# Optimization experiments

Measured on AMD Instinct MI355X. Metric: run time of the kernel, lower is better.

The kernel has to match this reference:

```python
import jax, jax.numpy as jnp
import numpy as np

C = 64          # number of concepts (output_size)
MC = 100        # num_monte_carlo
TRI = C * (C + 1) // 2
ROWS, COLS = np.tril_indices(C)          # static lower-triangular indices
DIAG_MASK = ROWS == COLS                 # positions in c_sigma that are diagonal
DIAG = np.arange(C)


def setup_inputs() -> dict:
    key = jax.random.key(0)
    k_x, k_eps, k_wmu, k_wsig = jax.random.split(key, 4)
    B, F = 4096, 512
    return {
        "x": jax.random.normal(k_x, (B, F), jnp.float32),
        "eps": jax.random.normal(k_eps, (B, C, MC), jnp.float32),  # MVN standard-normal draws
        "w_mu": jax.random.normal(k_wmu, (C, F), jnp.float32) / np.float32(np.sqrt(F)),
        "b_mu": jnp.zeros((C,), jnp.float32),
        # sigma.weight.data *= 0.01 in the original module
        "w_sigma": jax.random.normal(k_wsig, (TRI, F), jnp.float32) * np.float32(0.01 / np.sqrt(F)),
        "b_sigma": jnp.zeros((TRI,), jnp.float32),
    }


def reference(x, eps, w_mu, b_mu, w_sigma, b_sigma):
    # mu head: Linear(F -> C)
    c_mu = x @ w_mu.T + b_mu                          # [B, C]
    # sigma head: Linear(F -> C*(C+1)/2)
    c_sigma = x @ w_sigma.T + b_sigma                 # [B, TRI]

    B = x.shape[0]
    # build lower-triangular scale matrix (predict_sigma)
    L = jnp.zeros((B, C, C), x.dtype)
    L = L.at[:, ROWS, COLS].set(c_sigma)
    diag_vals = jax.nn.softplus(c_sigma[:, DIAG_MASK]) + 1e-6
    L = L.at[:, DIAG, DIAG].set(diag_vals)            # [B, C, C]

    # MVN rsample([MC]) with scale_tril L: sample = mu + L @ eps
    logits = c_mu[:, :, None] + jnp.einsum('bij,bjm->bim', L, eps)  # [B, C, MC]
    return jax.nn.sigmoid(logits)
```

## Files before the change

kernel.cpp:

```cpp
#include <hip/hip_runtime.h>
#include <hip/hip_bf16.h>


typedef short bf16x8 __attribute__((ext_vector_type(8)));
typedef float f32x4 __attribute__((ext_vector_type(4)));

__device__ __forceinline__ unsigned short f2bf(float f) {
    union { float f; unsigned u; } u; u.f = f;
    unsigned r = u.u + 0x7FFFu + ((u.u >> 16) & 1u);
    return (unsigned short)(r >> 16);
}

__device__ __forceinline__ void tri_ij(int t, int& i, int& j) {
    i = (int)((sqrtf((float)(8 * t + 1)) - 1.0f) * 0.5f);
    if ((i + 1) * (i + 2) / 2 <= t) ++i;
    if (i * (i + 1) / 2 > t) --i;
    j = t - ((i * (i + 1)) >> 1);
}

__device__ __forceinline__ void gload16(const void* g, void* l) {
    __builtin_amdgcn_global_load_lds(
        (const __attribute__((address_space(1))) void*)g,
        (__attribute__((address_space(3))) void*)l, 16, 0, 0);
}

__global__ __launch_bounds__(256) void cvt_kernel(
    const float* __restrict__ x, const float* __restrict__ wmu,
    const float* __restrict__ wsig,
    unsigned short* __restrict__ Xb, unsigned short* __restrict__ Wb,
    uint4* __restrict__ Ldz) {
    const int NX = (4096 * 512) / 4;
    const int NW = (2144 * 512) / 4;
    const int NMU = (64 * 512) / 4;
    const int NZ = (4096 * 64 * 64 * 2) / 16;
    int tot = NX + NW + NZ;
    for (int i = blockIdx.x * blockDim.x + threadIdx.x; i < tot;
         i += gridDim.x * blockDim.x) {
        if (i < NX + NW) {
            float4 v; unsigned short* dst;
            if (i < NX) {
                v = ((const float4*)x)[i];
                dst = Xb + (size_t)i * 4;
            } else {
                int j = i - NX;
                if (j < NMU) v = ((const float4*)wmu)[j];
                else         v = ((const float4*)wsig)[j - NMU];
                dst = Wb + (size_t)j * 4;
            }
            ushort4 o;
            o.x = f2bf(v.x); o.y = f2bf(v.y); o.z = f2bf(v.z); o.w = f2bf(v.w);
            *(ushort4*)dst = o;
        } else {
            Ldz[i - NX - NW] = make_uint4(0u, 0u, 0u, 0u);
        }
    }
}

__global__ __launch_bounds__(256) void gemm_kernel(
    const unsigned short* __restrict__ Xb, const unsigned short* __restrict__ Wb,
    const float* __restrict__ bmu, const float* __restrict__ bsig,
    float* __restrict__ Mu, unsigned short* __restrict__ Ld) {
    __shared__ __align__(16) unsigned short smem[16384];

    int flat = blockIdx.y * 17 + blockIdx.x;
    int virt = (flat & 7) * 68 + (flat >> 3);
    int vbx = virt % 17, vby = virt / 17;
    int r0 = vby * 128, c0 = vbx * 128;

    int tid = threadIdx.x;
    int w = tid >> 6, lane = tid & 63;
    int wr = w >> 1, wc = w & 1;
    int lr = lane & 15, kg = lane >> 4;

    int sr = tid >> 3;
    int sc = tid & 7;
    int scx = sc ^ (sr & 7);
    const unsigned short* Ag = Xb + (size_t)(r0 + sr) * 512 + scx * 8;
    const unsigned short* Bg = Wb + (size_t)(c0 + sr) * 512 + scx * 8;
    unsigned short* As = smem + tid * 8;
    unsigned short* Bs = smem + 8192 + tid * 8;

    f32x4 acc[4][4];
    #pragma unroll
    for (int i = 0; i < 4; ++i)
        #pragma unroll
        for (int j = 0; j < 4; ++j) acc[i][j] = (f32x4){0.f, 0.f, 0.f, 0.f};

    for (int kt = 0; kt < 8; ++kt) {
        int k0 = kt * 64;
        #pragma unroll
        for (int i = 0; i < 4; ++i) {
            gload16(Ag + (size_t)i * 32 * 512 + k0, As + i * 2048);
            gload16(Bg + (size_t)i * 32 * 512 + k0, Bs + i * 2048);
        }
        __syncthreads();
        #pragma unroll
        for (int h = 0; h < 2; ++h) {
            bf16x8 a[4], bv[4];
            #pragma unroll
            for (int i = 0; i < 4; ++i) {
                int row = wr * 64 + i * 16 + lr;
                int ch = ((h << 2) | kg) ^ (row & 7);
                a[i] = *(const bf16x8*)(smem + row * 64 + ch * 8);
            }
            #pragma unroll
            for (int j = 0; j < 4; ++j) {
                int row = wc * 64 + j * 16 + lr;
                int ch = ((h << 2) | kg) ^ (row & 7);
                bv[j] = *(const bf16x8*)(smem + 8192 + row * 64 + ch * 8);
            }
            #pragma unroll
            for (int i = 0; i < 4; ++i)
                #pragma unroll
                for (int j = 0; j < 4; ++j)
                    acc[i][j] = __builtin_amdgcn_mfma_f32_16x16x32_bf16(
                        a[i], bv[j], acc[i][j], 0, 0, 0);
        }
        __syncthreads();
    }

    int rbase = r0 + wr * 64 + (kg << 2);
    #pragma unroll
    for (int j = 0; j < 4; ++j) {
        int col = c0 + wc * 64 + j * 16 + lr;
        if (col < 64) {
            float bias = bmu[col];
            #pragma unroll
            for (int i = 0; i < 4; ++i)
                #pragma unroll
                for (int r = 0; r < 4; ++r)
                    Mu[(size_t)(rbase + i * 16 + r) * 64 + col] = acc[i][j][r] + bias;
        } else if (col < 2144) {
            int t = col - 64;
            float bias = bsig[t];
            int ti, tj; tri_ij(t, ti, tj);
            bool dg = (tj == ti);
            int ofs = ti * 64 + tj;
            #pragma unroll
            for (int i = 0; i < 4; ++i) {
                #pragma unroll
                for (int r = 0; r < 4; ++r) {
                    float v = acc[i][j][r] + bias;
                    if (dg) v = (v > 15.f ? v : __logf(1.f + __expf(v))) + 1e-6f;
                    Ld[((size_t)(rbase + i * 16 + r) << 12) + ofs] = f2bf(v);
                }
            }
        }
    }
}

__global__ __launch_bounds__(512, 4) void sample_kernel(
    const float* __restrict__ Mu, const unsigned short* __restrict__ Ld,
    const float* __restrict__ eps, float* __restrict__ out) {
    __shared__ __align__(16) float Ost[6400];

    int b = blockIdx.x;
    int tid = threadIdx.x;
    int w = tid >> 6, lane = tid & 63;
    int lr = lane & 15, kg = lane >> 4;
    int m = (w << 4) + lr;
    int ml = (m < 100) ? m : 96;
    int m0 = (w << 4) + (kg << 2);
    bool cw = (w < 7);
    bool st = cw && (m0 < 100);

    if (cw) {
        const float* er = eps + (size_t)b * 6400;
        float ef[16];
        #pragma unroll
        for (int s = 0; s < 8; ++s) {
            ef[s]     = er[(kg * 8 + s) * 100 + ml];
            ef[s + 8] = er[(32 + kg * 8 + s) * 100 + ml];
        }
        float muv[4];
        #pragma unroll
        for (int g = 0; g < 4; ++g)
            muv[g] = Mu[((size_t)b << 6) + g * 16 + lr];
        bf16x8 a0, a1;
        #pragma unroll
        for (int s = 0; s < 4; ++s) {
            __hip_bfloat162 h0 = __float22bfloat162_rn(
                make_float2(ef[2 * s], ef[2 * s + 1]));
            __hip_bfloat162 h1 = __float22bfloat162_rn(
                make_float2(ef[8 + 2 * s], ef[8 + 2 * s + 1]));
            ((unsigned*)&a0)[s] = *(unsigned*)&h0;
            ((unsigned*)&a1)[s] = *(unsigned*)&h1;
        }
        const unsigned short* lb = Ld + ((size_t)b << 12);
        #pragma unroll
        for (int g = 0; g < 4; ++g) {
            int i = g * 16 + lr;
            bf16x8 L0 = *(const bf16x8*)(lb + i * 64 + kg * 8);
            bf16x8 L1 = *(const bf16x8*)(lb + i * 64 + (kg + 4) * 8);
            f32x4 acc = {0.f, 0.f, 0.f, 0.f};
            acc = __builtin_amdgcn_mfma_f32_16x16x32_bf16(a0, L0, acc, 0, 0, 0);
            acc = __builtin_amdgcn_mfma_f32_16x16x32_bf16(a1, L1, acc, 0, 0, 0);
            if (st) {
                float4 o;
                #pragma unroll
                for (int r = 0; r < 4; ++r) {
                    float z = muv[g] + acc[r];
                    ((float*)&o)[r] = __fdividef(1.f, 1.f + __expf(-z));
                }
                *(float4*)&Ost[i * 100 + m0] = o;
            }
        }
    }

    __syncthreads();

    size_t ob = (size_t)b * 6400;
    #pragma unroll
    for (int kk = 0; kk < 4; ++kk) {
        int f = tid + (kk << 9);
        if (f < 1600)
            *(float4*)(out + ob + f * 4) = ((const float4*)Ost)[f];
    }
}

extern "C" void kernel_launch(void* const* d_in, const int* in_sizes, int n_in,
                              void* d_out, int out_size, void* d_ws, size_t ws_size,
                              hipStream_t stream) {
    const float* x    = (const float*)d_in[0];
    const float* eps  = (const float*)d_in[1];
    const float* wmu  = (const float*)d_in[2];
    const float* bmu  = (const float*)d_in[3];
    const float* wsig = (const float*)d_in[4];
    const float* bsig = (const float*)d_in[5];
    float* out = (float*)d_out;

    char* ws = (char*)d_ws;
    unsigned short* Xb = (unsigned short*)ws;
    unsigned short* Wb = (unsigned short*)(ws + 4194304);
    float*          Mu = (float*)(ws + 4194304 + 2195456);
    unsigned short* Ld = (unsigned short*)(ws + 7438336);

    cvt_kernel<<<2048, 256, 0, stream>>>(x, wmu, wsig, Xb, Wb, (uint4*)Ld);
    gemm_kernel<<<dim3(17, 32), 256, 0, stream>>>(Xb, Wb, bmu, bsig, Mu, Ld);
    sample_kernel<<<4096, 512, 0, stream>>>(Mu, Ld, eps, out);
}
```

Baseline: 94.58 us.

## Store packed triangular sigma and build L in LDS, batch four rows per block

Drops the dense zero-initialised 64x64 bf16 L buffer and instead writes the packed triangular sigma (2080 values per row) from the GEMM. The sample kernel stages the packed sigma and eps into LDS and expands L into MFMA fragments with masked reads. Each block now handles four batch rows in sequence with a swizzled grid mapping, which cuts the zero-fill and the dense L traffic. The costs are more LDS use, lower occupancy, and serial per-row loops with extra barriers.

```diff
diff --git a/kernel.cpp b/kernel.cpp
--- a/kernel.cpp
+++ b/kernel.cpp
@@ -10,6 +10,8 @@
     unsigned r = u.u + 0x7FFFu + ((u.u >> 16) & 1u);
     return (unsigned short)(r >> 16);
 }
+
+__device__ __forceinline__ int swz(int r) { return (r ^ (r >> 3)) & 7; }
 
 __device__ __forceinline__ void tri_ij(int t, int& i, int& j) {
     i = (int)((sqrtf((float)(8 * t + 1)) - 1.0f) * 0.5f);
@@ -27,39 +29,33 @@
 __global__ __launch_bounds__(256) void cvt_kernel(
     const float* __restrict__ x, const float* __restrict__ wmu,
     const float* __restrict__ wsig,
-    unsigned short* __restrict__ Xb, unsigned short* __restrict__ Wb,
-    uint4* __restrict__ Ldz) {
+    unsigned short* __restrict__ Xb, unsigned short* __restrict__ Wb) {
     const int NX = (4096 * 512) / 4;
     const int NW = (2144 * 512) / 4;
     const int NMU = (64 * 512) / 4;
-    const int NZ = (4096 * 64 * 64 * 2) / 16;
-    int tot = NX + NW + NZ;
+    int tot = NX + NW;
     for (int i = blockIdx.x * blockDim.x + threadIdx.x; i < tot;
          i += gridDim.x * blockDim.x) {
-        if (i < NX + NW) {
-            float4 v; unsigned short* dst;
-            if (i < NX) {
-                v = ((const float4*)x)[i];
-                dst = Xb + (size_t)i * 4;
-            } else {
-                int j = i - NX;
-                if (j < NMU) v = ((const float4*)wmu)[j];
-                else         v = ((const float4*)wsig)[j - NMU];
-                dst = Wb + (size_t)j * 4;
-            }
-            ushort4 o;
-            o.x = f2bf(v.x); o.y = f2bf(v.y); o.z = f2bf(v.z); o.w = f2bf(v.w);
-            *(ushort4*)dst = o;
+        float4 v; unsigned short* dst;
+        if (i < NX) {
+            v = ((const float4*)x)[i];
+            dst = Xb + (size_t)i * 4;
         } else {
-            Ldz[i - NX - NW] = make_uint4(0u, 0u, 0u, 0u);
-        }
+            int j = i - NX;
+            if (j < NMU) v = ((const float4*)wmu)[j];
+            else         v = ((const float4*)wsig)[j - NMU];
+            dst = Wb + (size_t)j * 4;
+        }
+        ushort4 o;
+        o.x = f2bf(v.x); o.y = f2bf(v.y); o.z = f2bf(v.z); o.w = f2bf(v.w);
+        *(ushort4*)dst = o;
     }
 }
 
 __global__ __launch_bounds__(256) void gemm_kernel(
     const unsigned short* __restrict__ Xb, const unsigned short* __restrict__ Wb,
     const float* __restrict__ bmu, const float* __restrict__ bsig,
-    float* __restrict__ Mu, unsigned short* __restrict__ Ld) {
+    float* __restrict__ Mu, unsigned short* __restrict__ Sg) {
     __shared__ __align__(16) unsigned short smem[16384];
 
     int flat = blockIdx.y * 17 + blockIdx.x;
@@ -135,86 +131,120 @@
             float bias = bsig[t];
             int ti, tj; tri_ij(t, ti, tj);
             bool dg = (tj == ti);
-            int ofs = ti * 64 + tj;
             #pragma unroll
             for (int i = 0; i < 4; ++i) {
                 #pragma unroll
                 for (int r = 0; r < 4; ++r) {
                     float v = acc[i][j][r] + bias;
                     if (dg) v = (v > 15.f ? v : __logf(1.f + __expf(v))) + 1e-6f;
-                    Ld[((size_t)(rbase + i * 16 + r) << 12) + ofs] = f2bf(v);
+                    Sg[(size_t)(rbase + i * 16 + r) * 2080 + t] = f2bf(v);
                 }
             }
         }
     }
 }
 
-__global__ __launch_bounds__(512, 4) void sample_kernel(
-    const float* __restrict__ Mu, const unsigned short* __restrict__ Ld,
+__global__ __launch_bounds__(512, 3) void sample_kernel(
+    const float* __restrict__ Mu, const unsigned short* __restrict__ Sg,
     const float* __restrict__ eps, float* __restrict__ out) {
+    __shared__ __align__(16) unsigned short EpT[112][64];
+    __shared__ __align__(16) unsigned short Sgs[2080];
     __shared__ __align__(16) float Ost[6400];
 
-    int b = blockIdx.x;
+    int flat = blockIdx.x;
+    int virt = (flat & 7) * 128 + (flat >> 3);
+    int b0 = virt << 2;
+
     int tid = threadIdx.x;
     int w = tid >> 6, lane = tid & 63;
     int lr = lane & 15, kg = lane >> 4;
-    int m = (w << 4) + lr;
-    int ml = (m < 100) ? m : 96;
+    bool cw = (w < 7);
     int m0 = (w << 4) + (kg << 2);
-    bool cw = (w < 7);
     bool st = cw && (m0 < 100);
-
-    if (cw) {
-        const float* er = eps + (size_t)b * 6400;
-        float ef[16];
-        #pragma unroll
-        for (int s = 0; s < 8; ++s) {
-            ef[s]     = er[(kg * 8 + s) * 100 + ml];
-            ef[s + 8] = er[(32 + kg * 8 + s) * 100 + ml];
-        }
-        float muv[4];
-        #pragma unroll
-        for (int g = 0; g < 4; ++g)
-            muv[g] = Mu[((size_t)b << 6) + g * 16 + lr];
-        bf16x8 a0, a1;
-        #pragma unroll
-        for (int s = 0; s < 4; ++s) {
-            __hip_bfloat162 h0 = __float22bfloat162_rn(
-                make_float2(ef[2 * s], ef[2 * s + 1]));
-            __hip_bfloat162 h1 = __float22bfloat162_rn(
-                make_float2(ef[8 + 2 * s], ef[8 + 2 * s + 1]));
-            ((unsigned*)&a0)[s] = *(unsigned*)&h0;
-            ((unsigned*)&a1)[s] = *(unsigned*)&h1;
-        }
-        const unsigned short* lb = Ld + ((size_t)b << 12);
-        #pragma unroll
-        for (int g = 0; g < 4; ++g) {
-            int i = g * 16 + lr;
-            bf16x8 L0 = *(const bf16x8*)(lb + i * 64 + kg * 8);
-            bf16x8 L1 = *(const bf16x8*)(lb + i * 64 + (kg + 4) * 8);
-            f32x4 acc = {0.f, 0.f, 0.f, 0.f};
-            acc = __builtin_amdgcn_mfma_f32_16x16x32_bf16(a0, L0, acc, 0, 0, 0);
-            acc = __builtin_amdgcn_mfma_f32_16x16x32_bf16(a1, L1, acc, 0, 0, 0);
-            if (st) {
-                float4 o;
-                #pragma unroll
-                for (int r = 0; r < 4; ++r) {
-                    float z = muv[g] + acc[r];
-                    ((float*)&o)[r] = __fdividef(1.f, 1.f + __expf(-z));
+    int mrow = (w << 4) + lr;
+    int mq = tid % 25, kq = tid / 25;
+
+    auto stage = [&](int b) {
+        if (tid < 260)
+            gload16(Sg + (size_t)b * 2080 + tid * 8, &Sgs[tid * 8]);
+        if (tid < 400) {
+            const float* p = eps + (size_t)b * 6400 + kq * 400 + mq * 4;
+            float4 v0 = *(const float4*)(p);
+            float4 v1 = *(const float4*)(p + 100);
+            float4 v2 = *(const float4*)(p + 200);
+            float4 v3 = *(const float4*)(p + 300);
+            #pragma unroll
+            for (int s = 0; s < 4; ++s) {
+                int m = (mq << 2) + s;
+                __hip_bfloat162 h0 = __float22bfloat162_rn(
+                    make_float2(((const float*)&v0)[s], ((const float*)&v1)[s]));
+                __hip_bfloat162 h1 = __float22bfloat162_rn(
+                    make_float2(((const float*)&v2)[s], ((const float*)&v3)[s]));
+                uint2 u; u.x = *(unsigned*)&h0; u.y = *(unsigned*)&h1;
+                int chunk = (kq >> 1) ^ swz(m);
+                *(uint2*)&EpT[m][(chunk << 3) | ((kq & 1) << 2)] = u;
+            }
+        }
+    };
+
+    stage(b0);
+    __syncthreads();
+
+    for (int k = 0; k < 4; ++k) {
+        int b = b0 + k;
+
+        if (cw) {
+            int smz = swz(mrow);
+            bf16x8 a0 = *(const bf16x8*)&EpT[mrow][(kg ^ smz) << 3];
+            bf16x8 a1 = *(const bf16x8*)&EpT[mrow][((kg + 4) ^ smz) << 3];
+            float muv[4];
+            #pragma unroll
+            for (int g = 0; g < 4; ++g)
+                muv[g] = Mu[((size_t)b << 6) + g * 16 + lr];
+            #pragma unroll
+            for (int g = 0; g < 4; ++g) {
+                int i = g * 16 + lr;
+                int t0 = (i * (i + 1)) >> 1;
+                bf16x8 L0, L1;
+                #pragma unroll
+                for (int s = 0; s < 4; ++s) {
+                    int ja = kg * 8 + 2 * s, jb = ja + 1;
+                    int jc = ja + 32,        jd = jb + 32;
+                    unsigned va = (ja <= i) ? (unsigned)Sgs[t0 + ja] : 0u;
+                    unsigned vb = (jb <= i) ? (unsigned)Sgs[t0 + jb] : 0u;
+                    ((unsigned*)&L0)[s] = va | (vb << 16);
+                    unsigned vc = (jc <= i) ? (unsigned)Sgs[t0 + jc] : 0u;
+                    unsigned vd = (jd <= i) ? (unsigned)Sgs[t0 + jd] : 0u;
+                    ((unsigned*)&L1)[s] = vc | (vd << 16);
                 }
-                *(float4*)&Ost[i * 100 + m0] = o;
-            }
-        }
-    }
-
-    __syncthreads();
-
-    size_t ob = (size_t)b * 6400;
-    #pragma unroll
-    for (int kk = 0; kk < 4; ++kk) {
-        int f = tid + (kk << 9);
-        if (f < 1600)
-            *(float4*)(out + ob + f * 4) = ((const float4*)Ost)[f];
+                f32x4 acc = {0.f, 0.f, 0.f, 0.f};
+                acc = __builtin_amdgcn_mfma_f32_16x16x32_bf16(a0, L0, acc, 0, 0, 0);
+                acc = __builtin_amdgcn_mfma_f32_16x16x32_bf16(a1, L1, acc, 0, 0, 0);
+                if (st) {
+                    float4 o;
+                    #pragma unroll
+                    for (int r = 0; r < 4; ++r) {
+                        float z = muv[g] + acc[r];
+                        ((float*)&o)[r] = __fdividef(1.f, 1.f + __expf(-z));
+                    }
+                    *(float4*)&Ost[i * 100 + m0] = o;
+                }
+            }
+        }
+
+        __syncthreads();
+
+        size_t ob = (size_t)b * 6400;
+        #pragma unroll
+        for (int kk = 0; kk < 4; ++kk) {
+            int f = tid + (kk << 9);
+            if (f < 1600)
+                *(float4*)(out + ob + f * 4) = ((const float4*)Ost)[f];
+        }
+
+        if (k < 3) stage(b + 1);
+
+        __syncthreads();
     }
 }
 
@@ -233,9 +263,9 @@
     unsigned short* Xb = (unsigned short*)ws;
     unsigned short* Wb = (unsigned short*)(ws + 4194304);
     float*          Mu = (float*)(ws + 4194304 + 2195456);
-    unsigned short* Ld = (unsigned short*)(ws + 7438336);
-
-    cvt_kernel<<<2048, 256, 0, stream>>>(x, wmu, wsig, Xb, Wb, (uint4*)Ld);
-    gemm_kernel<<<dim3(17, 32), 256, 0, stream>>>(Xb, Wb, bmu, bsig, Mu, Ld);
-    sample_kernel<<<4096, 512, 0, stream>>>(Mu, Ld, eps, out);
-}
+    unsigned short* Sg = (unsigned short*)(ws + 4194304 + 2195456 + 1048576);
+
+    cvt_kernel<<<2048, 256, 0, stream>>>(x, wmu, wsig, Xb, Wb);
+    gemm_kernel<<<dim3(17, 32), 256, 0, stream>>>(Xb, Wb, bmu, bsig, Mu, Sg);
+    sample_kernel<<<1024, 512, 0, stream>>>(Mu, Sg, eps, out);
+}
```

Result: faster. 80.99 us (-14.4%).
